# Performance work log

Hardware: AMD Instinct MI355X
Metric: run time of the kernel (lower is better)

The kernel has to match this reference:

```python
import jax, jax.numpy as jnp
import numpy as np

NPOS_MAX = 24  # npos_max
B, HEADS, H, W, HEAD_DIM = 8, 12, 24, 24, 64
SEQ = H * W


def setup_inputs() -> dict:
    key = jax.random.key(0)
    k1, k2, k3, k4 = jax.random.split(key, 4)
    # pos_emb params are zeros in torch init; randomized here so outputs/grads are nontrivial
    return {
        "query": jax.random.normal(k1, (B, HEADS, SEQ, HEAD_DIM), jnp.float32) * 0.1,
        "attn_logits": jax.random.normal(k2, (B, HEADS, SEQ, SEQ), jnp.float32),
        "pos_emb_x": jax.random.normal(k3, (HEAD_DIM, NPOS_MAX), jnp.float32) * 0.02,
        "pos_emb_y": jax.random.normal(k4, (HEAD_DIM, NPOS_MAX), jnp.float32) * 0.02,
        "wx": jnp.float32(0.5),
    }


def _cope_unit(query, attn_logits, pos_emb):
    # query: [N, heads, L, d]; attn_logits: [N, heads, L, L]; pos_emb: [d, npos]
    gates = jax.nn.sigmoid(attn_logits)
    pos = jnp.flip(jnp.cumsum(jnp.flip(gates, -1), axis=-1), -1)
    pos = jnp.minimum(pos, NPOS_MAX - 1)
    pos_ceil = jnp.ceil(pos).astype(jnp.int32)
    pos_floor = jnp.floor(pos).astype(jnp.int32)
    logits_int = jnp.einsum("nhld,dp->nhlp", query, pos_emb)  # [N,heads,L,npos]
    logits_ceil = jnp.take_along_axis(logits_int, pos_ceil, axis=-1)
    logits_floor = jnp.take_along_axis(logits_int, pos_floor, axis=-1)
    w = pos - pos_floor
    return logits_ceil * w + logits_floor * (1.0 - w)  # [N,heads,L,L]


def _cdist(x):
    # x: [BH, N, D] -> pairwise Euclidean distances [BH, N, N] (torch.cdist p=2)
    sq = jnp.sum(x * x, axis=-1)  # [BH, N]
    d2 = sq[:, :, None] + sq[:, None, :] - 2.0 * jnp.einsum("bnd,bmd->bnm", x, x)
    d2 = jnp.maximum(d2, 0.0)
    # safe sqrt: zero (not nan) gradient at identical points, matching torch.cdist
    return jnp.where(d2 > 0, jnp.sqrt(jnp.where(d2 > 0, d2, 1.0)), 0.0)


def reference(query, attn_logits, pos_emb_x, pos_emb_y, wx):
    b, heads, seq, d = query.shape
    h = w = int(np.sqrt(seq))
    q = query.reshape(b, heads, h, w, d)
    # row/column query slices (match torch permutes + reshapes)
    q_x = q.transpose(0, 2, 1, 3, 4).reshape(b * h, heads, w, d)
    q_y = q.transpose(0, 3, 1, 2, 4).reshape(b * w, heads, h, d)

    # vectorized replacement for the nested gather loops
    a = attn_logits.reshape(b, heads, h, w, h, w)
    # attn_x[b,h,i,j,k] = a[b,h,i,j,i,k]  -> diagonal over axes (2,4)
    attn_x = jnp.diagonal(a, axis1=2, axis2=4).transpose(0, 1, 4, 2, 3)  # [B,heads,H,W,W]
    # attn_y[b,h,i,j,k] = a[b,h,j,i,k,i]  -> diagonal over axes (3,5)
    attn_y = jnp.diagonal(a, axis1=3, axis2=5).transpose(0, 1, 4, 2, 3)  # [B,heads,W,H,H]

    # NOTE: faithful to the source's reshape (no permute) of [B,heads,H,W,W] -> [B*H,heads,W,W]
    attn_x_flat = attn_x.reshape(b * h, heads, w, w)
    attn_y_flat = attn_y.reshape(b * w, heads, h, h)

    w_x = _cope_unit(q_x, attn_x_flat, pos_emb_x).reshape(b, h, heads, w, w)
    w_y = _cope_unit(q_y, attn_y_flat, pos_emb_y).reshape(b, w, heads, h, h)

    # get_pe: flatten to [B*heads, H*W, W] / [B*heads, H*W, H] and take pairwise dists
    pe_x_flat = w_x.transpose(0, 2, 1, 3, 4).reshape(b * heads, h * w, w)
    pe_y_flat = w_y.transpose(0, 2, 3, 1, 4).reshape(b * heads, h * w, h)
    pe_res_x = _cdist(pe_x_flat).reshape(b, heads, h * w, h * w)
    pe_res_y = _cdist(pe_y_flat).reshape(b, heads, h * w, h * w)

    return wx * pe_res_x + (1.0 - wx) * pe_res_y
```

## Files before the change

### kernel.cpp

```cpp
#include <hip/hip_runtime.h>
#include <math.h>

#define NH 12
#define S 576
#define DD 64
#define P 24
#define NROWS 55296
#define GELEMS ((long)NROWS * P)
#define PSTRIDE 32

typedef unsigned int uint;
typedef unsigned short ushort;
typedef __bf16 bf16x8 __attribute__((ext_vector_type(8)));
typedef float f32x4 __attribute__((ext_vector_type(4)));

__device__ __forceinline__ uint bf16hi_bits(float v) {
    const uint u = __float_as_uint(v);
    return u + 0x7FFFu + ((u >> 16) & 1u);
}

__global__ __launch_bounds__(256) void gather_kernel(
    const float* __restrict__ attn, float* __restrict__ gx, float* __restrict__ gy)
{
    __shared__ float rb[16][580];
    const int tid = threadIdx.x;
    const int r0 = blockIdx.x * 16;
    const int hd = blockIdx.y, bb = blockIdx.z;
    const float4* src = (const float4*)(attn + ((long)(bb * NH + hd) * S + r0) * S);
    #pragma unroll
    for (int it = 0; it < 9; ++it) {
        const int i = it * 256 + tid;
        const int row = i / 144, c4 = i % 144;
        *(float4*)&rb[row][c4 * 4] = src[i];
    }
    __syncthreads();
    #pragma unroll
    for (int t = 0; t < 3; ++t) {
        const int e = t * 256 + tid;
        const int row = e / 48, jj = e % 48;
        const int r = r0 + row;
        const int band = r / 24, off = r % 24;
        if (jj < 24) {
            gx[((long)((bb * 288 + hd * 24 + band) * 24 + off)) * 24 + jj] =
                rb[row][band * 24 + jj];
        } else {
            const int k = jj - 24;
            gy[((long)((bb * 288 + hd * 24 + off) * 24 + band)) * 24 + k] =
                rb[row][k * 24 + off];
        }
    }
}

__global__ __launch_bounds__(256) void cope_kernel(
    const float* __restrict__ q,
    const float* __restrict__ gx, const float* __restrict__ gy,
    const float* __restrict__ Ex, const float* __restrict__ Ey,
    __bf16* __restrict__ pxh, __bf16* __restrict__ pxl,
    __bf16* __restrict__ pyh, __bf16* __restrict__ pyl,
    float* __restrict__ sqx, float* __restrict__ sqy)
{
    __shared__ float Et[24][68];
    __shared__ float Lr[32][28];
    __shared__ float Wr[32][28];

    const int tid = threadIdx.x;
    const int rl = tid >> 3, j = tid & 7;
    const int gidx0 = blockIdx.x * 32;
    const bool is_y = gidx0 >= NROWS;
    const int gu = gidx0 - (is_y ? NROWS : 0) + rl;

    const int l  = gu % 24;
    const int t2 = gu / 24;
    const int h  = t2 % NH, n = t2 / NH;
    const int bq = n / 24, oq = n % 24;
    const int qr = is_y ? (l * 24 + oq) : (oq * 24 + l);
    const int g  = bq * NH + h;

    const float* E = is_y ? Ey : Ex;
    for (int i = tid; i < 1536; i += 256) {
        const int d = i / 24, p = i % 24;
        Et[p][d] = E[i];
    }
    __syncthreads();

    const float* qrow = q + ((long)g * S + qr) * DD;
    float a0 = 0.f, a1 = 0.f, a2 = 0.f;
    const int p0 = j, p1 = j + 8, p2 = j + 16;
    #pragma unroll
    for (int d4 = 0; d4 < DD; d4 += 4) {
        const float4 qv = *(const float4*)(qrow + d4);
        const float4 e0 = *(const float4*)&Et[p0][d4];
        const float4 e1 = *(const float4*)&Et[p1][d4];
        const float4 e2 = *(const float4*)&Et[p2][d4];
        a0 = fmaf(qv.x, e0.x, fmaf(qv.y, e0.y, fmaf(qv.z, e0.z, fmaf(qv.w, e0.w, a0))));
        a1 = fmaf(qv.x, e1.x, fmaf(qv.y, e1.y, fmaf(qv.z, e1.z, fmaf(qv.w, e1.w, a1))));
        a2 = fmaf(qv.x, e2.x, fmaf(qv.y, e2.y, fmaf(qv.z, e2.z, fmaf(qv.w, e2.w, a2))));
    }
    Lr[rl][p0] = a0; Lr[rl][p1] = a1; Lr[rl][p2] = a2;
    __syncthreads();

    const float* grow = (is_y ? gy : gx) + (long)gu * P + 3 * j;
    float g0 = grow[0], g1 = grow[1], g2 = grow[2];
    g0 = 1.0f / (1.0f + __expf(-g0));
    g1 = 1.0f / (1.0f + __expf(-g1));
    g2 = 1.0f / (1.0f + __expf(-g2));
    const float s = g0 + g1 + g2;
    float T = s;
    #pragma unroll
    for (int d = 1; d < 8; d <<= 1) {
        const float o = __shfl_down(T, d, 8);
        T += (j + d < 8) ? o : 0.0f;
    }
    const float Exc = T - s;
    float posv[3];
    posv[0] = T;
    posv[1] = g1 + g2 + Exc;
    posv[2] = g2 + Exc;

    float sqp = 0.f;
    #pragma unroll
    for (int m = 0; m < 3; ++m) {
        const float pk  = fminf(posv[m], 23.0f);
        const float pf  = floorf(pk);
        const int   ic  = (int)ceilf(pk);
        const int   ifl = (int)pf;
        const float w   = pk - pf;
        const float o   = Lr[rl][ic] * w + Lr[rl][ifl] * (1.0f - w);
        Wr[rl][3 * j + m] = o;
        sqp += o * o;
    }
    #pragma unroll
    for (int d = 1; d < 8; d <<= 1) {
        const float o = __shfl_down(sqp, d, 8);
        sqp += (j + d < 8) ? o : 0.0f;
    }
    if (j == 0) (is_y ? sqy : sqx)[(long)g * S + qr] = sqp;
    __syncthreads();

    const int hl = tid >> 7, rem = tid & 127;
    const int r3 = rem >> 2, seg = rem & 3;
    const int gu3 = gidx0 - (is_y ? NROWS : 0) + r3;
    const int l3 = gu3 % 24, t23 = gu3 / 24;
    const int h3 = t23 % NH, n3 = t23 / NH;
    const int bq3 = n3 / 24, oq3 = n3 % 24;
    const int qr3 = is_y ? (l3 * 24 + oq3) : (oq3 * 24 + l3);
    const int g3 = bq3 * NH + h3;
    __bf16* dst = (is_y ? (hl ? pyl : pyh) : (hl ? pxl : pxh))
                  + ((long)g3 * S + qr3) * PSTRIDE + seg * 8;
    uint pk4[4] = {0u, 0u, 0u, 0u};
    if (seg < 3) {
        ushort hv[8];
        #pragma unroll
        for (int t = 0; t < 8; ++t) {
            const float o = Wr[r3][seg * 8 + t];
            const uint rh = bf16hi_bits(o);
            if (hl == 0) {
                hv[t] = (ushort)(rh >> 16);
            } else {
                const float hif = __uint_as_float(rh & 0xFFFF0000u);
                hv[t] = (ushort)(bf16hi_bits(o - hif) >> 16);
            }
        }
        #pragma unroll
        for (int t = 0; t < 4; ++t)
            pk4[t] = (uint)hv[2 * t] | ((uint)hv[2 * t + 1] << 16);
    }
    *(uint4*)dst = make_uint4(pk4[0], pk4[1], pk4[2], pk4[3]);
}

__global__ __launch_bounds__(256) void dist_kernel(
    const __bf16* __restrict__ pxh, const __bf16* __restrict__ pxl,
    const __bf16* __restrict__ pyh, const __bf16* __restrict__ pyl,
    const float* __restrict__ sqx, const float* __restrict__ sqy,
    const float* __restrict__ wxp, float* __restrict__ out)
{
    const int tid = threadIdx.x;
    const int w = tid >> 6, lane = tid & 63;
    const int til = blockIdx.x * 4 + w;
    if (til >= 81) return;
    const int g = blockIdx.y;
    const int tn = til / 9, tm = til % 9;
    const int lm = lane & 15, kg = lane >> 4;
    const float wx = wxp[0], wyc = 1.0f - wx;
    const long gb = (long)g * S;

    bf16x8 xbh[4], xbl[4], ybh[4], ybl[4];
    float smx[4], smy[4];
    #pragma unroll
    for (int nt = 0; nt < 4; ++nt) {
        const int row = tm * 64 + nt * 16 + lm;
        const long rb = (gb + row) * PSTRIDE + kg * 8;
        xbh[nt] = *(const bf16x8*)(pxh + rb);
        xbl[nt] = *(const bf16x8*)(pxl + rb);
        ybh[nt] = *(const bf16x8*)(pyh + rb);
        ybl[nt] = *(const bf16x8*)(pyl + rb);
        smx[nt] = sqx[gb + row];
        smy[nt] = sqy[gb + row];
    }

    #pragma unroll
    for (int mt = 0; mt < 4; ++mt) {
        const int arow = tn * 64 + mt * 16 + lm;
        const long ra = (gb + arow) * PSTRIDE + kg * 8;
        const bf16x8 xah = *(const bf16x8*)(pxh + ra);
        const bf16x8 xal = *(const bf16x8*)(pxl + ra);
        const bf16x8 yah = *(const bf16x8*)(pyh + ra);
        const bf16x8 yal = *(const bf16x8*)(pyl + ra);
        float snx[4], sny[4];
        #pragma unroll
        for (int rg = 0; rg < 4; ++rg) {
            const int r = tn * 64 + mt * 16 + kg * 4 + rg;
            snx[rg] = sqx[gb + r];
            sny[rg] = sqy[gb + r];
        }
        #pragma unroll
        for (int nt = 0; nt < 4; ++nt) {
            f32x4 ax = {0.f, 0.f, 0.f, 0.f};
            ax = __builtin_amdgcn_mfma_f32_16x16x32_bf16(xah, xbh[nt], ax, 0, 0, 0);
            ax = __builtin_amdgcn_mfma_f32_16x16x32_bf16(xah, xbl[nt], ax, 0, 0, 0);
            ax = __builtin_amdgcn_mfma_f32_16x16x32_bf16(xal, xbh[nt], ax, 0, 0, 0);
            f32x4 ay = {0.f, 0.f, 0.f, 0.f};
            ay = __builtin_amdgcn_mfma_f32_16x16x32_bf16(yah, ybh[nt], ay, 0, 0, 0);
            ay = __builtin_amdgcn_mfma_f32_16x16x32_bf16(yah, ybl[nt], ay, 0, 0, 0);
            ay = __builtin_amdgcn_mfma_f32_16x16x32_bf16(yal, ybh[nt], ay, 0, 0, 0);
            #pragma unroll
            for (int rg = 0; rg < 4; ++rg) {
                const int row = tn * 64 + mt * 16 + kg * 4 + rg;
                const int col = tm * 64 + nt * 16 + lm;
                const float d2x = fmaxf(fmaf(-2.0f, ax[rg], snx[rg] + smx[nt]), 0.0f);
                const float d2y = fmaxf(fmaf(-2.0f, ay[rg], sny[rg] + smy[nt]), 0.0f);
                const float dx = __builtin_amdgcn_sqrtf(d2x);
                const float dy = __builtin_amdgcn_sqrtf(d2y);
                out[(gb + row) * S + col] = fmaf(wx, dx, wyc * dy);
            }
        }
    }
}

extern "C" void kernel_launch(void* const* d_in, const int* in_sizes, int n_in,
                              void* d_out, int out_size, void* d_ws, size_t ws_size,
                              hipStream_t stream) {
    const float* q    = (const float*)d_in[0];
    const float* attn = (const float*)d_in[1];
    const float* Ex   = (const float*)d_in[2];
    const float* Ey   = (const float*)d_in[3];
    const float* wxp  = (const float*)d_in[4];
    float* out = (float*)d_out;

    float* gx = (float*)d_ws;
    float* gy = gx + GELEMS;
    __bf16* pxh = (__bf16*)(gy + GELEMS);
    __bf16* pxl = pxh + (long)NROWS * PSTRIDE;
    __bf16* pyh = pxl + (long)NROWS * PSTRIDE;
    __bf16* pyl = pyh + (long)NROWS * PSTRIDE;
    float* sqx = (float*)(pyl + (long)NROWS * PSTRIDE);
    float* sqy = sqx + NROWS;

    gather_kernel<<<dim3(36, NH, 8), 256, 0, stream>>>(attn, gx, gy);
    cope_kernel<<<3456, 256, 0, stream>>>(q, gx, gy, Ex, Ey,
                                          pxh, pxl, pyh, pyl, sqx, sqy);
    dist_kernel<<<dim3(21, 96), 256, 0, stream>>>(pxh, pxl, pyh, pyl,
                                                  sqx, sqy, wxp, out);
}
```

Measured before the change: 280.1 us.

## Fuse attention gather into CoPE kernel and flatten dist grid

Merges the gather kernel into the CoPE kernel, so each block loads a 16-row slab of attention logits into shared memory and reads its gate values for both x and y directly from there. This removes the gx/gy workspace round-trip and one kernel launch. The dist kernel is also launched on a flat 1D grid of exactly 81 tiles per group, so no waves are idle. The fused kernel uses more shared memory per block (about 45KB), which may lower occupancy, and its y-path gate reads from shared memory are strided.

```diff
diff --git a/kernel.cpp b/kernel.cpp
--- a/kernel.cpp
+++ b/kernel.cpp
@@ -6,7 +6,6 @@
 #define DD 64
 #define P 24
 #define NROWS 55296
-#define GELEMS ((long)NROWS * P)
 #define PSTRIDE 32
 
 typedef unsigned int uint;
@@ -19,88 +18,71 @@
     return u + 0x7FFFu + ((u >> 16) & 1u);
 }
 
-__global__ __launch_bounds__(256) void gather_kernel(
-    const float* __restrict__ attn, float* __restrict__ gx, float* __restrict__ gy)
-{
-    __shared__ float rb[16][580];
-    const int tid = threadIdx.x;
-    const int r0 = blockIdx.x * 16;
-    const int hd = blockIdx.y, bb = blockIdx.z;
-    const float4* src = (const float4*)(attn + ((long)(bb * NH + hd) * S + r0) * S);
-    #pragma unroll
-    for (int it = 0; it < 9; ++it) {
-        const int i = it * 256 + tid;
-        const int row = i / 144, c4 = i % 144;
-        *(float4*)&rb[row][c4 * 4] = src[i];
-    }
-    __syncthreads();
-    #pragma unroll
-    for (int t = 0; t < 3; ++t) {
-        const int e = t * 256 + tid;
-        const int row = e / 48, jj = e % 48;
-        const int r = r0 + row;
-        const int band = r / 24, off = r % 24;
-        if (jj < 24) {
-            gx[((long)((bb * 288 + hd * 24 + band) * 24 + off)) * 24 + jj] =
-                rb[row][band * 24 + jj];
-        } else {
-            const int k = jj - 24;
-            gy[((long)((bb * 288 + hd * 24 + off) * 24 + band)) * 24 + k] =
-                rb[row][k * 24 + off];
-        }
-    }
-}
-
-__global__ __launch_bounds__(256) void cope_kernel(
-    const float* __restrict__ q,
-    const float* __restrict__ gx, const float* __restrict__ gy,
+__global__ __launch_bounds__(256) void cope2_kernel(
+    const float* __restrict__ attn, const float* __restrict__ q,
     const float* __restrict__ Ex, const float* __restrict__ Ey,
     __bf16* __restrict__ pxh, __bf16* __restrict__ pxl,
     __bf16* __restrict__ pyh, __bf16* __restrict__ pyl,
     float* __restrict__ sqx, float* __restrict__ sqy)
 {
-    __shared__ float Et[24][68];
+    __shared__ float rb[16][580];
+    __shared__ float Et[2][24][68];
     __shared__ float Lr[32][28];
     __shared__ float Wr[32][28];
 
     const int tid = threadIdx.x;
-    const int rl = tid >> 3, j = tid & 7;
-    const int gidx0 = blockIdx.x * 32;
-    const bool is_y = gidx0 >= NROWS;
-    const int gu = gidx0 - (is_y ? NROWS : 0) + rl;
-
-    const int l  = gu % 24;
-    const int t2 = gu / 24;
-    const int h  = t2 % NH, n = t2 / NH;
+    const int r0 = blockIdx.x * 16;
+    const int hd = blockIdx.y, bb = blockIdx.z;
+
+    const float4* src = (const float4*)(attn + ((long)(bb * NH + hd) * S + r0) * S);
+    #pragma unroll
+    for (int it = 0; it < 9; ++it) {
+        const int i = it * 256 + tid;
+        *(float4*)&rb[i / 144][(i % 144) * 4] = src[i];
+    }
+    for (int i = tid; i < 1536; i += 256) {
+        const int d = i / 24, p = i % 24;
+        Et[0][p][d] = Ex[i];
+        Et[1][p][d] = Ey[i];
+    }
+    __syncthreads();
+
+    const int grp = tid >> 3, j = tid & 7;
+    const int is_y = grp >> 4;
+    const int rowloc = grp & 15;
+    const int r = r0 + rowloc;
+    const int a = r / 24, b = r % 24;
+    const int t2 = bb * 288 + hd * 24 + (is_y ? b : a);
+    const int l  = is_y ? a : b;
+    const int h  = t2 % 12, n = t2 / 12;
     const int bq = n / 24, oq = n % 24;
     const int qr = is_y ? (l * 24 + oq) : (oq * 24 + l);
-    const int g  = bq * NH + h;
-
-    const float* E = is_y ? Ey : Ex;
-    for (int i = tid; i < 1536; i += 256) {
-        const int d = i / 24, p = i % 24;
-        Et[p][d] = E[i];
-    }
-    __syncthreads();
-
-    const float* qrow = q + ((long)g * S + qr) * DD;
+    const int gm = bq * NH + h;
+
+    const float* qrow = q + ((long)gm * S + qr) * DD;
     float a0 = 0.f, a1 = 0.f, a2 = 0.f;
-    const int p0 = j, p1 = j + 8, p2 = j + 16;
     #pragma unroll
     for (int d4 = 0; d4 < DD; d4 += 4) {
         const float4 qv = *(const float4*)(qrow + d4);
-        const float4 e0 = *(const float4*)&Et[p0][d4];
-        const float4 e1 = *(const float4*)&Et[p1][d4];
-        const float4 e2 = *(const float4*)&Et[p2][d4];
+        const float4 e0 = *(const float4*)&Et[is_y][j][d4];
+        const float4 e1 = *(const float4*)&Et[is_y][j + 8][d4];
+        const float4 e2 = *(const float4*)&Et[is_y][j + 16][d4];
         a0 = fmaf(qv.x, e0.x, fmaf(qv.y, e0.y, fmaf(qv.z, e0.z, fmaf(qv.w, e0.w, a0))));
         a1 = fmaf(qv.x, e1.x, fmaf(qv.y, e1.y, fmaf(qv.z, e1.z, fmaf(qv.w, e1.w, a1))));
         a2 = fmaf(qv.x, e2.x, fmaf(qv.y, e2.y, fmaf(qv.z, e2.z, fmaf(qv.w, e2.w, a2))));
     }
-    Lr[rl][p0] = a0; Lr[rl][p1] = a1; Lr[rl][p2] = a2;
-    __syncthreads();
-
-    const float* grow = (is_y ? gy : gx) + (long)gu * P + 3 * j;
-    float g0 = grow[0], g1 = grow[1], g2 = grow[2];
+    Lr[grp][j] = a0; Lr[grp][j + 8] = a1; Lr[grp][j + 16] = a2;
+
+    float g0, g1, g2;
+    if (is_y) {
+        g0 = rb[rowloc][(3 * j + 0) * 24 + b];
+        g1 = rb[rowloc][(3 * j + 1) * 24 + b];
+        g2 = rb[rowloc][(3 * j + 2) * 24 + b];
+    } else {
+        g0 = rb[rowloc][a * 24 + 3 * j + 0];
+        g1 = rb[rowloc][a * 24 + 3 * j + 1];
+        g2 = rb[rowloc][a * 24 + 3 * j + 2];
+    }
     g0 = 1.0f / (1.0f + __expf(-g0));
     g1 = 1.0f / (1.0f + __expf(-g1));
     g2 = 1.0f / (1.0f + __expf(-g2));
@@ -125,8 +107,8 @@
         const int   ic  = (int)ceilf(pk);
         const int   ifl = (int)pf;
         const float w   = pk - pf;
-        const float o   = Lr[rl][ic] * w + Lr[rl][ifl] * (1.0f - w);
-        Wr[rl][3 * j + m] = o;
+        const float o   = Lr[grp][ic] * w + Lr[grp][ifl] * (1.0f - w);
+        Wr[grp][3 * j + m] = o;
         sqp += o * o;
     }
     #pragma unroll
@@ -134,25 +116,28 @@
         const float o = __shfl_down(sqp, d, 8);
         sqp += (j + d < 8) ? o : 0.0f;
     }
-    if (j == 0) (is_y ? sqy : sqx)[(long)g * S + qr] = sqp;
+    if (j == 0) (is_y ? sqy : sqx)[(long)gm * S + qr] = sqp;
     __syncthreads();
 
     const int hl = tid >> 7, rem = tid & 127;
-    const int r3 = rem >> 2, seg = rem & 3;
-    const int gu3 = gidx0 - (is_y ? NROWS : 0) + r3;
-    const int l3 = gu3 % 24, t23 = gu3 / 24;
-    const int h3 = t23 % NH, n3 = t23 / NH;
+    const int grp3 = rem >> 2, seg = rem & 3;
+    const int is_y3 = grp3 >> 4;
+    const int r3 = r0 + (grp3 & 15);
+    const int a3 = r3 / 24, b3 = r3 % 24;
+    const int t23 = bb * 288 + hd * 24 + (is_y3 ? b3 : a3);
+    const int l3  = is_y3 ? a3 : b3;
+    const int h3  = t23 % 12, n3 = t23 / 12;
     const int bq3 = n3 / 24, oq3 = n3 % 24;
-    const int qr3 = is_y ? (l3 * 24 + oq3) : (oq3 * 24 + l3);
-    const int g3 = bq3 * NH + h3;
-    __bf16* dst = (is_y ? (hl ? pyl : pyh) : (hl ? pxl : pxh))
-                  + ((long)g3 * S + qr3) * PSTRIDE + seg * 8;
+    const int qr3 = is_y3 ? (l3 * 24 + oq3) : (oq3 * 24 + l3);
+    const int gm3 = bq3 * NH + h3;
+    __bf16* dst = (is_y3 ? (hl ? pyl : pyh) : (hl ? pxl : pxh))
+                  + ((long)gm3 * S + qr3) * PSTRIDE + seg * 8;
     uint pk4[4] = {0u, 0u, 0u, 0u};
     if (seg < 3) {
         ushort hv[8];
         #pragma unroll
         for (int t = 0; t < 8; ++t) {
-            const float o = Wr[r3][seg * 8 + t];
+            const float o = Wr[grp3][seg * 8 + t];
             const uint rh = bf16hi_bits(o);
             if (hl == 0) {
                 hv[t] = (ushort)(rh >> 16);
@@ -175,11 +160,11 @@
     const float* __restrict__ wxp, float* __restrict__ out)
 {
     const int tid = threadIdx.x;
-    const int w = tid >> 6, lane = tid & 63;
-    const int til = blockIdx.x * 4 + w;
-    if (til >= 81) return;
-    const int g = blockIdx.y;
-    const int tn = til / 9, tm = til % 9;
+    const int lane = tid & 63;
+    const int tg = blockIdx.x * 4 + (tid >> 6);
+    const int g = tg / 81;
+    const int til = tg - g * 81;
+    const int tn = til / 9, tm = til - tn * 9;
     const int lm = lane & 15, kg = lane >> 4;
     const float wx = wxp[0], wyc = 1.0f - wx;
     const long gb = (long)g * S;
@@ -209,9 +194,9 @@
         float snx[4], sny[4];
         #pragma unroll
         for (int rg = 0; rg < 4; ++rg) {
-            const int r = tn * 64 + mt * 16 + kg * 4 + rg;
-            snx[rg] = sqx[gb + r];
-            sny[rg] = sqy[gb + r];
+            const int rr = tn * 64 + mt * 16 + kg * 4 + rg;
+            snx[rg] = sqx[gb + rr];
+            sny[rg] = sqy[gb + rr];
         }
         #pragma unroll
         for (int nt = 0; nt < 4; ++nt) {
@@ -247,18 +232,15 @@
     const float* wxp  = (const float*)d_in[4];
     float* out = (float*)d_out;
 
-    float* gx = (float*)d_ws;
-    float* gy = gx + GELEMS;
-    __bf16* pxh = (__bf16*)(gy + GELEMS);
+    __bf16* pxh = (__bf16*)d_ws;
     __bf16* pxl = pxh + (long)NROWS * PSTRIDE;
     __bf16* pyh = pxl + (long)NROWS * PSTRIDE;
     __bf16* pyl = pyh + (long)NROWS * PSTRIDE;
     float* sqx = (float*)(pyl + (long)NROWS * PSTRIDE);
     float* sqy = sqx + NROWS;
 
-    gather_kernel<<<dim3(36, NH, 8), 256, 0, stream>>>(attn, gx, gy);
-    cope_kernel<<<3456, 256, 0, stream>>>(q, gx, gy, Ex, Ey,
-                                          pxh, pxl, pyh, pyl, sqx, sqy);
-    dist_kernel<<<dim3(21, 96), 256, 0, stream>>>(pxh, pxl, pyh, pyl,
-                                                  sqx, sqy, wxp, out);
-}
+    cope2_kernel<<<dim3(36, NH, 8), 256, 0, stream>>>(
+        attn, q, Ex, Ey, pxh, pxl, pyh, pyl, sqx, sqy);
+    dist_kernel<<<1944, 256, 0, stream>>>(pxh, pxl, pyh, pyl,
+                                          sqx, sqy, wxp, out);
+}
```

Measured after the change: 280.4 us. About the same (+0.1%).
